# Performance work log

Measured on AMD Instinct MI355X. Metric: run time of the kernel, lower is better.

The kernel has to match this reference:

```python
import jax, jax.numpy as jnp
import numpy as np

B, N, D = 8, 1024, 768
NHEAD = 4
N_EDGES = 3
ITERS = 2
DK = D // NHEAD


def setup_inputs() -> dict:
    key = jax.random.key(0)
    ks = jax.random.split(key, 12)
    s = 0.02
    return {
        "nodes_embed": jax.random.normal(ks[0], (B, N, D), dtype=jnp.float32),
        "node_adj": jax.random.randint(ks[1], (B, N, N), 0, 4, dtype=jnp.int32),
        # per-edge-type Q/K linear layers (torch Linear: y = x W^T + b; stored here as [in,out])
        "Wq": jax.random.normal(ks[2], (N_EDGES, D, D), dtype=jnp.float32) * s,
        "bq": jax.random.normal(ks[3], (N_EDGES, D), dtype=jnp.float32) * s,
        "Wk": jax.random.normal(ks[4], (N_EDGES, D, D), dtype=jnp.float32) * s,
        "bk": jax.random.normal(ks[5], (N_EDGES, D), dtype=jnp.float32) * s,
        # GCN weights: shared across heads (self.blocks reuses the same Sequential), distinct per iter
        "gcn_W": jax.random.normal(ks[6], (ITERS, D, D), dtype=jnp.float32) * s,
        "gcn_b": jnp.zeros((ITERS, D), dtype=jnp.float32),
        # aggregate_W: Linear(D*nhead -> D), stored as [D*nhead, D]
        "W_agg": jax.random.normal(ks[7], (D * NHEAD, D), dtype=jnp.float32) * s,
        "b_agg": jnp.zeros((D,), dtype=jnp.float32),
    }


def reference(nodes_embed, node_adj, Wq, bq, Wk, bk, gcn_W, gcn_b, W_agg, b_agg):
    Bv, Nv, Dv = nodes_embed.shape
    h, dk = NHEAD, DK
    adj = node_adj[:, None, :, :]  # [B,1,N,N]
    scale = 1.0 / jnp.sqrt(jnp.asarray(dk, nodes_embed.dtype))

    scores = jnp.zeros((Bv, h, Nv, Nv), dtype=nodes_embed.dtype)
    for e in range(N_EDGES):  # small fixed edge-type loop
        q = (nodes_embed @ Wq[e] + bq[e]).reshape(Bv, Nv, h, dk).transpose(0, 2, 1, 3)  # [B,h,N,dk]
        k = (nodes_embed @ Wk[e] + bk[e]).reshape(Bv, Nv, h, dk).transpose(0, 2, 1, 3)
        s = jnp.einsum('bhnd,bhmd->bhnm', q, k) * scale
        scores = scores + jnp.where(adj == e + 1, s, jnp.zeros((), s.dtype))
    scores = jnp.where(scores == 0, jnp.asarray(-1e9, scores.dtype), scores)
    attn = jax.nn.softmax(scores, axis=-1)          # [B,h,N,N]
    ga = jnp.transpose(attn, (1, 0, 2, 3))          # [h,B,N,N]

    # GCN blocks, vectorized over heads; weights shared across heads
    X = jnp.broadcast_to(nodes_embed, (h, Bv, Nv, Dv))  # [h,B,N,D]
    for i in range(ITERS):
        H = jnp.einsum('hbnd,de->hbne', X, gcn_W[i])
        sum_nei = jnp.einsum('hbnm,hbmd->hbnd', ga, H)
        degs = jnp.sum(ga, axis=-1, keepdims=True)       # [h,B,N,1]
        dst = sum_nei / degs + gcn_b[i]
        X = X + jax.nn.relu(dst)

    # torch.cat over heads along feature dim -> [B,N,h*D]
    cat = jnp.transpose(X, (1, 2, 0, 3)).reshape(Bv, Nv, h * Dv)
    out = cat @ W_agg + b_agg
    return out, ga
```

## Files before the change

### kernel.cpp

```cpp
#include <hip/hip_runtime.h>

typedef long long i64;
typedef unsigned short u16;
typedef __attribute__((ext_vector_type(8))) short short8;
typedef __attribute__((ext_vector_type(4))) float f32x4;

#define Bv 8
#define Nv 1024
#define Dv 768
#define Hh 4
#define DKv 192
#define BND ((i64)Bv * Nv * Dv)
#define HBND ((i64)Hh * BND)

__device__ __forceinline__ u16 f2bf(float f) {
    unsigned u = __builtin_bit_cast(unsigned, f);
    u += 0x7fffu + ((u >> 16) & 1u);
    return (u16)(u >> 16);
}
__device__ __forceinline__ float bf2f(u16 h) {
    unsigned u = ((unsigned)h) << 16;
    return __builtin_bit_cast(float, u);
}

__device__ __forceinline__ void gl_lds16(const u16* g, u16* l) {
    __builtin_amdgcn_global_load_lds(
        (const __attribute__((address_space(1))) void*)g,
        (__attribute__((address_space(3))) void*)l, 16, 0, 0);
}

template <int EPI, bool CATK, int ORD, int NBN, int NBM, int NZ>
__global__ __launch_bounds__(256) void gemm_bf16(
    const u16* __restrict__ A, i64 sA, int lda,
    const u16* __restrict__ Bt, i64 sBt, int ldbt,
    const float* __restrict__ bias, i64 sBias, const float* __restrict__ bias2,
    void* __restrict__ Cv, i64 sC, int ldc, int K, int koff)
{
    __shared__ u16 Asb[128 * 64];
    __shared__ u16 Bsb[128 * 64];

    const int L = (blockIdx.x & 7) * ((NBN * NBM * NZ) >> 3) + (blockIdx.x >> 3);
    int bn, bm, z;
    if (ORD == 0) {
        bn = L % NBN; const int t2 = L / NBN; bm = t2 % NBM; z = t2 / NBM;
    } else {
        bn = L % NBN; const int t2 = L / NBN; z = t2 % NZ; bm = t2 / NZ;
    }

    A  += (i64)z * sA;
    Bt += (i64)z * sBt;
    const float* bp = bias;
    int zb = z;
    if (bias2 != nullptr && z >= NZ / 2) { bp = bias2; zb = z - NZ / 2; }
    if (bp) bp += (i64)zb * sBias;
    const int kb = z * koff;

    const int bmp = bm * 128, bnp = bn * 128;
    const int tid = threadIdx.x;
    const int w = tid >> 6, l = tid & 63;
    const int wr = w >> 1, wc = w & 1;
    const int kgrp = l >> 4, lr = l & 15;

    const u16* Ab = A + (i64)bmp * lda;
    const u16* Bb = Bt + (i64)bnp * ldbt;

    f32x4 acc[4][4];
    #pragma unroll
    for (int i = 0; i < 4; ++i)
        #pragma unroll
        for (int j = 0; j < 4; ++j)
            acc[i][j] = (f32x4){0.f, 0.f, 0.f, 0.f};

    for (int k0i = 0; k0i < K; k0i += 64) {
        const int k0 = kb + k0i;
        if (k0i) __syncthreads();
        #pragma unroll
        for (int t = 0; t < 4; ++t) {
            const int idx = t * 256 + tid;
            const int r = idx >> 3, s = idx & 7;
            const int ss = s ^ (r & 7);
            const u16* src;
            if (CATK) {
                src = A + (i64)(k0 / Dv) * BND + (i64)(bmp + r) * Dv + (k0 % Dv) + ss * 8;
            } else {
                src = Ab + (i64)r * lda + k0 + ss * 8;
            }
            gl_lds16(src, &Asb[(t * 256 + w * 64) * 8]);
        }
        #pragma unroll
        for (int t = 0; t < 4; ++t) {
            const int idx = t * 256 + tid;
            const int r = idx >> 3, s = idx & 7;
            const int ss = s ^ (r & 7);
            gl_lds16(Bb + (i64)r * ldbt + k0 + ss * 8, &Bsb[(t * 256 + w * 64) * 8]);
        }
        __syncthreads();

        #pragma unroll
        for (int ks = 0; ks < 2; ++ks) {
            const int slot = ks * 4 + kgrp;
            short8 a[4], b[4];
            #pragma unroll
            for (int i = 0; i < 4; ++i) {
                const int r = wc * 64 + i * 16 + lr;
                a[i] = *(const short8*)&Bsb[r * 64 + ((slot ^ (r & 7)) << 3)];
            }
            #pragma unroll
            for (int j = 0; j < 4; ++j) {
                const int r = wr * 64 + j * 16 + lr;
                b[j] = *(const short8*)&Asb[r * 64 + ((slot ^ (r & 7)) << 3)];
            }
            #pragma unroll
            for (int i = 0; i < 4; ++i)
                #pragma unroll
                for (int j = 0; j < 4; ++j)
                    acc[i][j] = __builtin_amdgcn_mfma_f32_16x16x32_bf16(
                        a[i], b[j], acc[i][j], 0, 0, 0);
        }
    }

    f32x4 bj[4];
    #pragma unroll
    for (int i = 0; i < 4; ++i) {
        const int nb = bnp + wc * 64 + i * 16 + kgrp * 4;
        bj[i] = bp ? *(const f32x4*)&bp[nb] : (f32x4){0.f, 0.f, 0.f, 0.f};
    }

    #pragma unroll
    for (int j = 0; j < 4; ++j) {
        const int m = bmp + wr * 64 + j * 16 + lr;
        #pragma unroll
        for (int i = 0; i < 4; ++i) {
            const int nb = bnp + wc * 64 + i * 16 + kgrp * 4;
            const i64 off = (i64)z * sC + (i64)m * ldc + nb;
            f32x4 v = acc[i][j] + bj[i];
            if (EPI == 0) {
                *(f32x4*)&((float*)Cv)[off] = v;
            } else if (EPI == 1) {
                ushort4 o;
                o.x = f2bf(v[0]); o.y = f2bf(v[1]);
                o.z = f2bf(v[2]); o.w = f2bf(v[3]);
                *(ushort4*)&((u16*)Cv)[off] = o;
            } else {
                u16* xp = (u16*)Cv + off;
                ushort4 old = *(const ushort4*)xp;
                ushort4 o;
                o.x = f2bf(bf2f(old.x) + fmaxf(v[0], 0.f));
                o.y = f2bf(bf2f(old.y) + fmaxf(v[1], 0.f));
                o.z = f2bf(bf2f(old.z) + fmaxf(v[2], 0.f));
                o.w = f2bf(bf2f(old.w) + fmaxf(v[3], 0.f));
                *(ushort4*)xp = o;
            }
        }
    }
}

__global__ __launch_bounds__(256) void scores_mfma(
    const u16* __restrict__ qb, const u16* __restrict__ kb,
    const int* __restrict__ adj, u16* __restrict__ sb)
{
    __shared__ u16 Qs[2][64 * 64];
    __shared__ u16 Ks[2][64 * 64];

    const int bid = blockIdx.x;
    const int b = bid & 7;
    const int t2 = bid >> 3;
    const int h = t2 & 3;
    const int mt = (t2 >> 2) & 15;
    const int nt = t2 >> 6;
    const int m0 = mt * 64, n0 = nt * 64;
    const int zga = h * 8 + b;

    const int tid = threadIdx.x;
    const int w = tid >> 6, l = tid & 63;
    const int wr = w >> 1, wc = w & 1;
    const int kgrp = l >> 4, lr = l & 15;

    const i64 qoff = ((i64)b * Nv + n0) * Dv + h * DKv;
    const i64 koff = ((i64)b * Nv + m0) * Dv + h * DKv;

#define STAGE_SC(ci_, buf_) { \
    const int e_ = (ci_) / 3, k0_ = ((ci_) % 3) * 64; \
    const u16* qe_ = qb + (i64)e_ * BND + qoff; \
    const u16* ke_ = kb + (i64)e_ * BND + koff; \
    _Pragma("unroll") \
    for (int t = 0; t < 2; ++t) { \
        const int idx2 = t * 256 + tid; \
        const int r = idx2 >> 3, s = idx2 & 7; \
        const int ss = s ^ (r & 7); \
        gl_lds16(qe_ + (i64)r * Dv + k0_ + ss * 8, &Qs[buf_][(t * 256 + w * 64) * 8]); \
        gl_lds16(ke_ + (i64)r * Dv + k0_ + ss * 8, &Ks[buf_][(t * 256 + w * 64) * 8]); \
    } }

    int4 adjv[2][2];
    #pragma unroll
    for (int i = 0; i < 2; ++i) {
        const int mb = m0 + wc * 32 + i * 16 + kgrp * 4;
        #pragma unroll
        for (int j = 0; j < 2; ++j) {
            const int n = n0 + wr * 32 + j * 16 + lr;
            adjv[i][j] = *(const int4*)&adj[((i64)b * Nv + n) * Nv + mb];
        }
    }

    f32x4 acc[3][2][2];
    #pragma unroll
    for (int e = 0; e < 3; ++e)
        #pragma unroll
        for (int i = 0; i < 2; ++i)
            #pragma unroll
            for (int j = 0; j < 2; ++j)
                acc[e][i][j] = (f32x4){0.f, 0.f, 0.f, 0.f};

    STAGE_SC(0, 0)

    #pragma unroll
    for (int ci = 0; ci < 9; ++ci) {
        const int cur = ci & 1;
        if (ci < 8) {
            if (cur) { STAGE_SC(ci + 1, 0) } else { STAGE_SC(ci + 1, 1) }
            asm volatile("s_waitcnt vmcnt(4)" ::: "memory");
        } else {
            asm volatile("s_waitcnt vmcnt(0)" ::: "memory");
        }
        __builtin_amdgcn_s_barrier();
        asm volatile("" ::: "memory");

        const int e = ci / 3;
        #pragma unroll
        for (int ks = 0; ks < 2; ++ks) {
            const int slot = ks * 4 + kgrp;
            short8 a[2], bq2[2];
            #pragma unroll
            for (int i = 0; i < 2; ++i) {
                const int r = wc * 32 + i * 16 + lr;
                a[i] = *(const short8*)&Ks[cur][r * 64 + ((slot ^ (r & 7)) << 3)];
            }
            #pragma unroll
            for (int j = 0; j < 2; ++j) {
                const int r = wr * 32 + j * 16 + lr;
                bq2[j] = *(const short8*)&Qs[cur][r * 64 + ((slot ^ (r & 7)) << 3)];
            }
            #pragma unroll
            for (int i = 0; i < 2; ++i)
                #pragma unroll
                for (int j = 0; j < 2; ++j)
                    acc[e][i][j] = __builtin_amdgcn_mfma_f32_16x16x32_bf16(
                        a[i], bq2[j], acc[e][i][j], 0, 0, 0);
        }

        asm volatile("s_waitcnt lgkmcnt(0)" ::: "memory");
        __builtin_amdgcn_s_barrier();
    }
#undef STAGE_SC

    const float scale = 0.07216878364870323f;
    #pragma unroll
    for (int i = 0; i < 2; ++i) {
        const int mb = m0 + wc * 32 + i * 16 + kgrp * 4;
        #pragma unroll
        for (int j = 0; j < 2; ++j) {
            const int n = n0 + wr * 32 + j * 16 + lr;
            const int av[4] = {adjv[i][j].x, adjv[i][j].y, adjv[i][j].z, adjv[i][j].w};
            ushort4 o;
            #pragma unroll
            for (int rg = 0; rg < 4; ++rg) {
                float f = 0.f;
                if (av[rg] == 1) f = acc[0][i][j][rg];
                else if (av[rg] == 2) f = acc[1][i][j][rg];
                else if (av[rg] == 3) f = acc[2][i][j][rg];
                f *= scale;
                if (f == 0.f) f = -1e9f;
                ((u16*)&o)[rg] = f2bf(f);
            }
            *(ushort4*)&sb[((i64)zga * Nv + n) * Nv + mb] = o;
        }
    }
}

__global__ __launch_bounds__(256) void softmax_k(const u16* __restrict__ sb,
                                                 float* __restrict__ ga,
                                                 u16* __restrict__ gab)
{
    const i64 row = blockIdx.x;
    const int tid = threadIdx.x;
    const int wid = tid >> 6, lane = tid & 63;

    ushort4 sv = *(const ushort4*)&sb[row * (i64)Nv + tid * 4];
    float4 v;
    v.x = bf2f(sv.x); v.y = bf2f(sv.y); v.z = bf2f(sv.z); v.w = bf2f(sv.w);

    float m = fmaxf(fmaxf(v.x, v.y), fmaxf(v.z, v.w));
    #pragma unroll
    for (int o = 32; o >= 1; o >>= 1) m = fmaxf(m, __shfl_xor(m, o));

    __shared__ float red[4];
    if (lane == 0) red[wid] = m;
    __syncthreads();
    m = fmaxf(fmaxf(red[0], red[1]), fmaxf(red[2], red[3]));

    float e0 = expf(v.x - m), e1 = expf(v.y - m), e2 = expf(v.z - m), e3 = expf(v.w - m);
    float s = e0 + e1 + e2 + e3;
    #pragma unroll
    for (int o = 32; o >= 1; o >>= 1) s += __shfl_xor(s, o);
    __syncthreads();
    if (lane == 0) red[wid] = s;
    __syncthreads();
    s = red[0] + red[1] + red[2] + red[3];

    const float inv = 1.0f / s;
    float4 o;
    o.x = e0 * inv; o.y = e1 * inv; o.z = e2 * inv; o.w = e3 * inv;
    *(float4*)&ga[row * (i64)Nv + tid * 4] = o;

    ushort4 ob;
    ob.x = f2bf(o.x); ob.y = f2bf(o.y); ob.z = f2bf(o.z); ob.w = f2bf(o.w);
    *(ushort4*)&gab[row * (i64)Nv + tid * 4] = ob;
}

__global__ __launch_bounds__(256) void prep_k(const float* __restrict__ nodes,
                                              u16* __restrict__ nodesb,
                                              u16* __restrict__ Xb)
{
    const i64 i = (i64)blockIdx.x * 256 + threadIdx.x;
    float4 v = ((const float4*)nodes)[i];
    ushort4 o;
    o.x = f2bf(v.x); o.y = f2bf(v.y); o.z = f2bf(v.z); o.w = f2bf(v.w);
    ((ushort4*)nodesb)[i] = o;
    const i64 q4 = BND / 4;
    #pragma unroll
    for (int h = 0; h < Hh; ++h) ((ushort4*)Xb)[(i64)h * q4 + i] = o;
}

__global__ __launch_bounds__(256) void trans_all(
    const float* __restrict__ Wq, const float* __restrict__ Wk,
    const float* __restrict__ gcnW, const float* __restrict__ Wagg,
    u16* __restrict__ wqkt, u16* __restrict__ gcnWt, u16* __restrict__ waggt)
{
    const int z = blockIdx.z;
    const i64 W768 = (i64)768 * 768;
    const float* src;
    u16* dst;
    int ldo;
    if (z < 3)      { src = Wq + z * W768;        dst = wqkt + z * W768;          ldo = 768; }
    else if (z < 6) { src = Wk + (z - 3) * W768;  dst = wqkt + (i64)z * W768;     ldo = 768; }
    else if (z < 8) { src = gcnW + (z - 6) * W768; dst = gcnWt + (i64)(z - 6) * W768; ldo = 768; }
    else            { src = Wagg + (i64)(z - 8) * W768; dst = waggt + (i64)(z - 8) * 768; ldo = 3072; }

    __shared__ u16 t[32][33];
    const int c0 = blockIdx.x * 32, r0 = blockIdx.y * 32;
    const int tx = threadIdx.x & 31, ty = threadIdx.x >> 5;
    #pragma unroll
    for (int i = ty; i < 32; i += 8)
        t[i][tx] = f2bf(src[(i64)(r0 + i) * 768 + c0 + tx]);
    __syncthreads();
    #pragma unroll
    for (int i = ty; i < 32; i += 8)
        dst[(i64)(c0 + i) * ldo + r0 + tx] = t[tx][i];
}

__global__ __launch_bounds__(256) void addbias_k(
    const float* __restrict__ p0, const float* __restrict__ p1,
    const float* __restrict__ bias, float* __restrict__ out)
{
    const i64 i4 = (i64)blockIdx.x * 256 + threadIdx.x;
    const int nb = (int)((i4 * 4) % Dv);
    float4 a = ((const float4*)p0)[i4];
    float4 b = ((const float4*)p1)[i4];
    float4 bv = *(const float4*)&bias[nb];
    float4 o;
    o.x = a.x + b.x + bv.x; o.y = a.y + b.y + bv.y;
    o.z = a.z + b.z + bv.z; o.w = a.w + b.w + bv.w;
    ((float4*)out)[i4] = o;
}

extern "C" void kernel_launch(void* const* d_in, const int* in_sizes, int n_in,
                              void* d_out, int out_size, void* d_ws, size_t ws_size,
                              hipStream_t stream)
{
    const float* nodes = (const float*)d_in[0];
    const int*   adj   = (const int*)d_in[1];
    const float* Wq    = (const float*)d_in[2];
    const float* bq    = (const float*)d_in[3];
    const float* Wk    = (const float*)d_in[4];
    const float* bk    = (const float*)d_in[5];
    const float* gcnW  = (const float*)d_in[6];
    const float* gcnb  = (const float*)d_in[7];
    const float* Wagg  = (const float*)d_in[8];
    const float* bagg  = (const float*)d_in[9];

    float* out = (float*)d_out;
    float* gaf = out + BND;

    const i64 W768 = (i64)768 * 768;
    u16* ws     = (u16*)d_ws;
    u16* qb     = ws;
    u16* kb2    = ws + 3 * BND;
    u16* gab    = ws;
    u16* nodesb = ws + 6 * BND;
    u16* gcnWt  = nodesb + BND;
    u16* waggt  = gcnWt + 2 * W768;
    u16* Xb     = waggt + 4 * W768;
    u16* Htb    = Xb + HBND;
    u16* wqkt   = Htb;
    u16* sbuf   = Htb;
    float* part = (float*)Htb;

    dim3 blk(256);

    prep_k<<<dim3((unsigned)(BND / 4 / 256)), blk, 0, stream>>>(nodes, nodesb, Xb);
    trans_all<<<dim3(24, 24, 12), blk, 0, stream>>>(Wq, Wk, gcnW, Wagg, wqkt, gcnWt, waggt);

    gemm_bf16<1, false, 1, 6, 64, 6><<<dim3(2304), blk, 0, stream>>>(
        nodesb, 0, Dv, wqkt, W768, Dv, bq, Dv, bk, qb, BND, Dv, Dv, 0);

    scores_mfma<<<dim3(8192), blk, 0, stream>>>(qb, kb2, adj, sbuf);

    softmax_k<<<dim3(Hh * Bv * Nv), blk, 0, stream>>>(sbuf, gaf, gab);

    for (int it = 0; it < 2; ++it) {
        gemm_bf16<1, false, 0, 256, 6, 1><<<dim3(1536), blk, 0, stream>>>(
            gcnWt + (i64)it * W768, 0, Dv, Xb, 0, Dv, nullptr, 0, nullptr,
            Htb, 0, 32768, Dv, 0);
        gemm_bf16<2, false, 0, 6, 8, 32><<<dim3(1536), blk, 0, stream>>>(
            gab, (i64)Nv * Nv, Nv, Htb, 1024, 32768, gcnb + (i64)it * Dv, 0, nullptr,
            Xb, (i64)Nv * Dv, Dv, Nv, 0);
    }

    gemm_bf16<0, true, 0, 6, 64, 2><<<dim3(768), blk, 0, stream>>>(
        Xb, 0, Dv, waggt, 0, Hh * Dv, nullptr, 0, nullptr,
        part, BND, Dv, (Hh * Dv) / 2, (Hh * Dv) / 2);

    addbias_k<<<dim3((unsigned)(BND / 4 / 256)), blk, 0, stream>>>(
        part, part + BND, bagg, out);
}
```

Before: 574.6 us.

## Enlarge scores tile along N and skip redundant per-head first GCN projection

The scores kernel now computes a 64x128 tile per block instead of 64x64. Each block loads twice as many Q rows, so each K tile is reused across more outputs, and the grid halves. The adjacency values are loaded in the epilogue rather than prefetched, and launch bounds request 3 waves per SIMD. In the first GCN iteration all heads share the same input X, so the projection runs once on the node embeddings rather than four times, and the aggregation GEMM broadcasts that shared H across heads through a new z-mask on the B operand. This adds register pressure in the scores kernel.

```diff
diff --git a/kernel.cpp b/kernel.cpp
--- a/kernel.cpp
+++ b/kernel.cpp
@@ -32,7 +32,7 @@
 template <int EPI, bool CATK, int ORD, int NBN, int NBM, int NZ>
 __global__ __launch_bounds__(256) void gemm_bf16(
     const u16* __restrict__ A, i64 sA, int lda,
-    const u16* __restrict__ Bt, i64 sBt, int ldbt,
+    const u16* __restrict__ Bt, i64 sBt, int ldbt, int zmaskBt,
     const float* __restrict__ bias, i64 sBias, const float* __restrict__ bias2,
     void* __restrict__ Cv, i64 sC, int ldc, int K, int koff)
 {
@@ -48,7 +48,7 @@
     }
 
     A  += (i64)z * sA;
-    Bt += (i64)z * sBt;
+    Bt += (i64)(z & zmaskBt) * sBt;
     const float* bp = bias;
     int zb = z;
     if (bias2 != nullptr && z >= NZ / 2) { bp = bias2; zb = z - NZ / 2; }
@@ -155,11 +155,11 @@
     }
 }
 
-__global__ __launch_bounds__(256) void scores_mfma(
+__global__ __launch_bounds__(256, 3) void scores_mfma(
     const u16* __restrict__ qb, const u16* __restrict__ kb,
     const int* __restrict__ adj, u16* __restrict__ sb)
 {
-    __shared__ u16 Qs[2][64 * 64];
+    __shared__ u16 Qs[2][128 * 64];
     __shared__ u16 Ks[2][64 * 64];
 
     const int bid = blockIdx.x;
@@ -168,12 +168,12 @@
     const int h = t2 & 3;
     const int mt = (t2 >> 2) & 15;
     const int nt = t2 >> 6;
-    const int m0 = mt * 64, n0 = nt * 64;
+    const int m0 = mt * 64, n0 = nt * 128;
     const int zga = h * 8 + b;
 
     const int tid = threadIdx.x;
     const int w = tid >> 6, l = tid & 63;
-    const int wr = w >> 1, wc = w & 1;
+    const int wn = w >> 1, wm = w & 1;
     const int kgrp = l >> 4, lr = l & 15;
 
     const i64 qoff = ((i64)b * Nv + n0) * Dv + h * DKv;
@@ -184,32 +184,27 @@
     const u16* qe_ = qb + (i64)e_ * BND + qoff; \
     const u16* ke_ = kb + (i64)e_ * BND + koff; \
     _Pragma("unroll") \
+    for (int t = 0; t < 4; ++t) { \
+        const int idx2 = t * 256 + tid; \
+        const int r = idx2 >> 3, s = idx2 & 7; \
+        const int ss = s ^ (r & 7); \
+        gl_lds16(qe_ + (i64)r * Dv + k0_ + ss * 8, &Qs[buf_][(t * 256 + w * 64) * 8]); \
+    } \
+    _Pragma("unroll") \
     for (int t = 0; t < 2; ++t) { \
         const int idx2 = t * 256 + tid; \
         const int r = idx2 >> 3, s = idx2 & 7; \
         const int ss = s ^ (r & 7); \
-        gl_lds16(qe_ + (i64)r * Dv + k0_ + ss * 8, &Qs[buf_][(t * 256 + w * 64) * 8]); \
         gl_lds16(ke_ + (i64)r * Dv + k0_ + ss * 8, &Ks[buf_][(t * 256 + w * 64) * 8]); \
     } }
 
-    int4 adjv[2][2];
-    #pragma unroll
-    for (int i = 0; i < 2; ++i) {
-        const int mb = m0 + wc * 32 + i * 16 + kgrp * 4;
-        #pragma unroll
-        for (int j = 0; j < 2; ++j) {
-            const int n = n0 + wr * 32 + j * 16 + lr;
-            adjv[i][j] = *(const int4*)&adj[((i64)b * Nv + n) * Nv + mb];
-        }
-    }
-
-    f32x4 acc[3][2][2];
+    f32x4 acc[3][2][4];
     #pragma unroll
     for (int e = 0; e < 3; ++e)
         #pragma unroll
         for (int i = 0; i < 2; ++i)
             #pragma unroll
-            for (int j = 0; j < 2; ++j)
+            for (int j = 0; j < 4; ++j)
                 acc[e][i][j] = (f32x4){0.f, 0.f, 0.f, 0.f};
 
     STAGE_SC(0, 0)
@@ -219,7 +214,7 @@
         const int cur = ci & 1;
         if (ci < 8) {
             if (cur) { STAGE_SC(ci + 1, 0) } else { STAGE_SC(ci + 1, 1) }
-            asm volatile("s_waitcnt vmcnt(4)" ::: "memory");
+            asm volatile("s_waitcnt vmcnt(6)" ::: "memory");
         } else {
             asm volatile("s_waitcnt vmcnt(0)" ::: "memory");
         }
@@ -230,21 +225,21 @@
         #pragma unroll
         for (int ks = 0; ks < 2; ++ks) {
             const int slot = ks * 4 + kgrp;
-            short8 a[2], bq2[2];
+            short8 a[2], bq2[4];
             #pragma unroll
             for (int i = 0; i < 2; ++i) {
-                const int r = wc * 32 + i * 16 + lr;
+                const int r = wm * 32 + i * 16 + lr;
                 a[i] = *(const short8*)&Ks[cur][r * 64 + ((slot ^ (r & 7)) << 3)];
             }
             #pragma unroll
-            for (int j = 0; j < 2; ++j) {
-                const int r = wr * 32 + j * 16 + lr;
+            for (int j = 0; j < 4; ++j) {
+                const int r = wn * 64 + j * 16 + lr;
                 bq2[j] = *(const short8*)&Qs[cur][r * 64 + ((slot ^ (r & 7)) << 3)];
             }
             #pragma unroll
             for (int i = 0; i < 2; ++i)
                 #pragma unroll
-                for (int j = 0; j < 2; ++j)
+                for (int j = 0; j < 4; ++j)
                     acc[e][i][j] = __builtin_amdgcn_mfma_f32_16x16x32_bf16(
                         a[i], bq2[j], acc[e][i][j], 0, 0, 0);
         }
@@ -257,11 +252,12 @@
     const float scale = 0.07216878364870323f;
     #pragma unroll
     for (int i = 0; i < 2; ++i) {
-        const int mb = m0 + wc * 32 + i * 16 + kgrp * 4;
-        #pragma unroll
-        for (int j = 0; j < 2; ++j) {
-            const int n = n0 + wr * 32 + j * 16 + lr;
-            const int av[4] = {adjv[i][j].x, adjv[i][j].y, adjv[i][j].z, adjv[i][j].w};
+        const int mb = m0 + wm * 32 + i * 16 + kgrp * 4;
+        #pragma unroll
+        for (int j = 0; j < 4; ++j) {
+            const int n = n0 + wn * 64 + j * 16 + lr;
+            const int4 adjv = *(const int4*)&adj[((i64)b * Nv + n) * Nv + mb];
+            const int av[4] = {adjv.x, adjv.y, adjv.z, adjv.w};
             ushort4 o;
             #pragma unroll
             for (int rg = 0; rg < 4; ++rg) {
@@ -412,23 +408,32 @@
     trans_all<<<dim3(24, 24, 12), blk, 0, stream>>>(Wq, Wk, gcnW, Wagg, wqkt, gcnWt, waggt);
 
     gemm_bf16<1, false, 1, 6, 64, 6><<<dim3(2304), blk, 0, stream>>>(
-        nodesb, 0, Dv, wqkt, W768, Dv, bq, Dv, bk, qb, BND, Dv, Dv, 0);
-
-    scores_mfma<<<dim3(8192), blk, 0, stream>>>(qb, kb2, adj, sbuf);
+        nodesb, 0, Dv, wqkt, W768, Dv, -1, bq, Dv, bk, qb, BND, Dv, Dv, 0);
+
+    scores_mfma<<<dim3(4096), blk, 0, stream>>>(qb, kb2, adj, sbuf);
 
     softmax_k<<<dim3(Hh * Bv * Nv), blk, 0, stream>>>(sbuf, gaf, gab);
 
     for (int it = 0; it < 2; ++it) {
-        gemm_bf16<1, false, 0, 256, 6, 1><<<dim3(1536), blk, 0, stream>>>(
-            gcnWt + (i64)it * W768, 0, Dv, Xb, 0, Dv, nullptr, 0, nullptr,
-            Htb, 0, 32768, Dv, 0);
-        gemm_bf16<2, false, 0, 6, 8, 32><<<dim3(1536), blk, 0, stream>>>(
-            gab, (i64)Nv * Nv, Nv, Htb, 1024, 32768, gcnb + (i64)it * Dv, 0, nullptr,
-            Xb, (i64)Nv * Dv, Dv, Nv, 0);
+        if (it == 0) {
+            gemm_bf16<1, false, 0, 64, 6, 1><<<dim3(384), blk, 0, stream>>>(
+                gcnWt, 0, Dv, nodesb, 0, Dv, -1, nullptr, 0, nullptr,
+                Htb, 0, 8192, Dv, 0);
+            gemm_bf16<2, false, 0, 6, 8, 32><<<dim3(1536), blk, 0, stream>>>(
+                gab, (i64)Nv * Nv, Nv, Htb, 1024, 8192, 7, gcnb, 0, nullptr,
+                Xb, (i64)Nv * Dv, Dv, Nv, 0);
+        } else {
+            gemm_bf16<1, false, 0, 256, 6, 1><<<dim3(1536), blk, 0, stream>>>(
+                gcnWt + W768, 0, Dv, Xb, 0, Dv, -1, nullptr, 0, nullptr,
+                Htb, 0, 32768, Dv, 0);
+            gemm_bf16<2, false, 0, 6, 8, 32><<<dim3(1536), blk, 0, stream>>>(
+                gab, (i64)Nv * Nv, Nv, Htb, 1024, 32768, -1, gcnb + (i64)Dv, 0, nullptr,
+                Xb, (i64)Nv * Dv, Dv, Nv, 0);
+        }
     }
 
     gemm_bf16<0, true, 0, 6, 64, 2><<<dim3(768), blk, 0, stream>>>(
-        Xb, 0, Dv, waggt, 0, Hh * Dv, nullptr, 0, nullptr,
+        Xb, 0, Dv, waggt, 0, Hh * Dv, -1, nullptr, 0, nullptr,
         part, BND, Dv, (Hh * Dv) / 2, (Hh * Dv) / 2);
 
     addbias_k<<<dim3((unsigned)(BND / 4 / 256)), blk, 0, stream>>>(
```

Measured after the change: 550.9 us. 4.1% less time.
